# Kernel tuning notes

Hardware: AMD Instinct MI355X
Metric: run time of the kernel (lower is better)

Reference implementation:

```python
import jax, jax.numpy as jnp
import numpy as np

B, F, H, D, K = 16384, 4096, 512, 64, 512  # batch, feat, hidden, emb_dim, codebook size
M = H // D  # code positions per sample


def _leaky(h):
    return jnp.where(h > 0, h, 0.01 * h)


def setup_inputs() -> dict:
    key = jax.random.key(0)
    ks = jax.random.split(key, 16)
    lin = lambda k, i, o: jax.random.normal(k, (i, o), jnp.float32) * (1.0 / np.sqrt(i))
    return {
        "x": jax.random.uniform(ks[0], (B, F), jnp.float32),
        "We1": lin(ks[1], F, 256), "be1": jnp.zeros((256,), jnp.float32),
        "We2": lin(ks[2], 256, 128), "be2": jnp.zeros((128,), jnp.float32),
        "We3": lin(ks[3], 128, H), "be3": jnp.zeros((H,), jnp.float32),
        "Wd1": lin(ks[4], H, 128), "bd1": jnp.zeros((128,), jnp.float32),
        "Wd2": lin(ks[5], 128, 256), "bd2": jnp.zeros((256,), jnp.float32),
        "Wd3": lin(ks[6], 256, F), "bd3": jnp.zeros((F,), jnp.float32),
        "codebook": jax.random.normal(ks[7], (D, K), jnp.float32) * 0.02,  # (emb_dim, num_embeddings)
    }


def _nearest(z_e, codebook):
    # z_e: (B, D, M); codebook: (D, K). Squared-distance argmin over K.
    x2 = jnp.sum(z_e * z_e, axis=1)                       # (B, M)
    xw = jnp.einsum('bdm,dk->bmk', z_e, codebook)         # (B, M, K)
    w2 = jnp.sum(codebook * codebook, axis=0)             # (K,)
    idx = jnp.argmin(x2[..., None] - 2.0 * xw + w2, axis=-1)  # (B, M)
    quant = jnp.swapaxes(codebook.T[idx], 1, 2)           # (B, D, M)
    return quant, idx


def reference(x, We1, be1, We2, be2, We3, be3, Wd1, bd1, Wd2, bd2, Wd3, bd3, codebook):
    # encoder MLP
    h = _leaky(x @ We1 + be1)
    h = _leaky(h @ We2 + be2)
    h = _leaky(h @ We3 + be3)                             # (B, H)
    z_e = h.reshape(B, D, M)
    # emb(z_e, weight_sg=True): straight-through, weight detached
    quant_sg, idx = _nearest(z_e, jax.lax.stop_gradient(codebook))
    z_q = z_e + jax.lax.stop_gradient(quant_sg - z_e)
    # emb(z_e.detach()): grads (if any) flow to codebook via gather
    emb, _ = _nearest(jax.lax.stop_gradient(z_e), codebook)
    # decoder MLP
    g = _leaky(z_q.reshape(B, H) @ Wd1 + bd1)
    g = _leaky(g @ Wd2 + bd2)
    X_pred = jax.nn.sigmoid(g @ Wd3 + bd3)                # (B, F)
    return idx, z_e, z_q, emb, X_pred
```

## Files before the change

kernel.cpp:

```cpp
#include <hip/hip_runtime.h>
#include <cstdint>
#include <cstddef>


static constexpr int BB = 16384;

typedef __attribute__((ext_vector_type(8))) short short8;
typedef __attribute__((ext_vector_type(8))) _Float16 half8;
typedef __attribute__((ext_vector_type(4))) float f32x4;

__device__ __forceinline__ unsigned short f2bf(float f) {
    union { float f; uint32_t u; } v; v.f = f;
    uint32_t r = (v.u + 0x7FFFu + ((v.u >> 16) & 1u)) >> 16;
    return (unsigned short)r;
}

__device__ __forceinline__ void lds_barrier() {
    asm volatile("s_waitcnt lgkmcnt(0)" ::: "memory");
    __builtin_amdgcn_s_barrier();
    __builtin_amdgcn_sched_barrier(0);
}

__global__ __launch_bounds__(256) void combine_act(
    const float* __restrict__ part, int S, size_t MN,
    const float* __restrict__ bias, int N,
    float* __restrict__ outF)
{
    const size_t e = ((size_t)blockIdx.x * 256 + threadIdx.x) * 4;
    if (e >= MN) return;
    float4 s = *(const float4*)(part + e);
    for (int i = 1; i < S; i++) {
        const float4 p = *(const float4*)(part + (size_t)i * MN + e);
        s.x += p.x; s.y += p.y; s.z += p.z; s.w += p.w;
    }
    const int col = (int)(e & (size_t)(N - 1));
    const float4 bv = *(const float4*)(bias + col);
    float v0 = s.x + bv.x, v1 = s.y + bv.y, v2 = s.z + bv.z, v3 = s.w + bv.w;
    v0 = (v0 > 0.f) ? v0 : 0.01f * v0;
    v1 = (v1 > 0.f) ? v1 : 0.01f * v1;
    v2 = (v2 > 0.f) ? v2 : 0.01f * v2;
    v3 = (v3 > 0.f) ? v3 : 0.01f * v3;
    float4 o; o.x = v0; o.y = v1; o.z = v2; o.w = v3;
    *(float4*)(outF + e) = o;
}

__global__ __launch_bounds__(256) void transpose_cast(
    const float* __restrict__ W, unsigned short* __restrict__ WT, int R, int Cc)
{
    __shared__ float s[32][33];
    const int tx = threadIdx.x & 31, ty = threadIdx.x >> 5;
    const int c0 = blockIdx.x * 32, r0 = blockIdx.y * 32;
#pragma unroll
    for (int i = 0; i < 4; i++)
        s[ty + i * 8][tx] = W[(size_t)(r0 + ty + i * 8) * Cc + c0 + tx];
    __syncthreads();
#pragma unroll
    for (int i = 0; i < 4; i++)
        WT[(size_t)(c0 + ty + i * 8) * R + r0 + tx] = f2bf(s[tx][ty + i * 8]);
}

__global__ __launch_bounds__(256) void transpose_split_f16(
    const float* __restrict__ W, unsigned short* __restrict__ Th,
    unsigned short* __restrict__ Tl, int R, int Cc)
{
    __shared__ float s[32][33];
    const int tx = threadIdx.x & 31, ty = threadIdx.x >> 5;
    const int c0 = blockIdx.x * 32, r0 = blockIdx.y * 32;
#pragma unroll
    for (int i = 0; i < 4; i++)
        s[ty + i * 8][tx] = W[(size_t)(r0 + ty + i * 8) * Cc + c0 + tx];
    __syncthreads();
#pragma unroll
    for (int i = 0; i < 4; i++) {
        const float f = s[tx][ty + i * 8];
        const _Float16 h = (_Float16)f;
        const float fh = (float)h;
        const _Float16 lo = (_Float16)((f - fh) * 4096.0f);
        union { _Float16 hf; unsigned short u; } ch, cl;
        ch.hf = h; cl.hf = lo;
        Th[(size_t)(c0 + ty + i * 8) * R + r0 + tx] = ch.u;
        Tl[(size_t)(c0 + ty + i * 8) * R + r0 + tx] = cl.u;
    }
}

template<int BUF>
__device__ __forceinline__ void enc1_step(
    int K0,
    const float* __restrict__ gA,
    const unsigned short* __restrict__ gBh,
    const unsigned short* __restrict__ gBl,
    short (&Ah)[2][2048], short (&Al)[2][2048],
    half8 (&bhC)[4], half8 (&bhN)[4], half8 (&blS)[4],
    f32x4& p0, f32x4& p1,
    f32x4 (&acc1)[4][4], f32x4 (&acc2)[4][4],
    int aoff, int fr0)
{
    constexpr size_t rstep = (size_t)16 * 4096;
    const int kn1 = K0 + 32, kn2 = K0 + 64;
    lds_barrier();
#pragma unroll
    for (int j = 0; j < 4; j++)
        blS[j] = *(const half8*)(gBl + (size_t)j * rstep + K0);
    if (kn1 < 2048) {
#pragma unroll
        for (int j = 0; j < 4; j++)
            bhN[j] = *(const half8*)(gBh + (size_t)j * rstep + kn1);
    }
    f32x4 f0, f1;
    if (kn2 < 2048) {
        f0 = __builtin_nontemporal_load((const f32x4*)(gA + kn2));
        f1 = __builtin_nontemporal_load((const f32x4*)(gA + kn2 + 4));
    }
    half8 ah[4];
#pragma unroll
    for (int i = 0; i < 4; i++)
        ah[i] = *(const half8*)&Ah[BUF][(i << 9) + fr0];
#pragma unroll
    for (int i = 0; i < 4; i++)
#pragma unroll
        for (int j = 0; j < 4; j++)
            acc1[i][j] = __builtin_amdgcn_mfma_f32_16x16x32_f16(
                ah[i], bhC[j], acc1[i][j], 0, 0, 0);
#pragma unroll
    for (int i = 0; i < 4; i++)
#pragma unroll
        for (int j = 0; j < 4; j++)
            acc2[i][j] = __builtin_amdgcn_mfma_f32_16x16x32_f16(
                ah[i], blS[j], acc2[i][j], 0, 0, 0);
    half8 al[4];
#pragma unroll
    for (int i = 0; i < 4; i++)
        al[i] = *(const half8*)&Al[BUF][(i << 9) + fr0];
#pragma unroll
    for (int i = 0; i < 4; i++)
#pragma unroll
        for (int j = 0; j < 4; j++)
            acc2[i][j] = __builtin_amdgcn_mfma_f32_16x16x32_f16(
                al[i], bhC[j], acc2[i][j], 0, 0, 0);
    if (kn1 < 2048) {
        float fv[8];
        *(f32x4*)&fv[0] = p0;
        *(f32x4*)&fv[4] = p1;
        union { _Float16 h[8]; short8 s; } uh, ul;
#pragma unroll
        for (int e = 0; e < 8; e++) {
            const float f = fv[e];
            const _Float16 h = (_Float16)f;
            const float fh = (float)h;
            uh.h[e] = h;
            ul.h[e] = (_Float16)((f - fh) * 4096.0f);
        }
        *(short8*)&Ah[BUF ^ 1][aoff] = uh.s;
        *(short8*)&Al[BUF ^ 1][aoff] = ul.s;
    }
    if (kn2 < 2048) { p0 = f0; p1 = f1; }
}

__global__ __launch_bounds__(256, 2) void gemm_f16x2_enc1(
    const float* __restrict__ X,
    const unsigned short* __restrict__ Bh,
    const unsigned short* __restrict__ Bl,
    float* __restrict__ part)
{
    __shared__ short Ah[2][2048];
    __shared__ short Al[2][2048];
    const int tid = threadIdx.x;
    const int l = tid & 63, w = tid >> 6;
    const int lm = l & 15, lq = l >> 4;
    const int bm = blockIdx.y * 64;
    const int kStart = blockIdx.z * 2048;

    const float* gA = X + (size_t)(bm + w * 16 + lm) * 4096 + kStart + lq * 8;
    const unsigned short* gBh = Bh + (size_t)(w * 64 + lm) * 4096 + kStart + lq * 8;
    const unsigned short* gBl = Bl + (size_t)(w * 64 + lm) * 4096 + kStart + lq * 8;
    constexpr size_t rstep = (size_t)16 * 4096;

    const int aoff = (w << 9) + (l << 3);
    const int fr0 = (lq << 7) + (lm << 3);

    f32x4 acc1[4][4], acc2[4][4];
#pragma unroll
    for (int i = 0; i < 4; i++)
#pragma unroll
        for (int j = 0; j < 4; j++) {
            acc1[i][j] = (f32x4){0.f, 0.f, 0.f, 0.f};
            acc2[i][j] = (f32x4){0.f, 0.f, 0.f, 0.f};
        }

    half8 bhA[4], bhB[4], blS[4];
    f32x4 p0, p1;

    {
#pragma unroll
        for (int j = 0; j < 4; j++)
            bhA[j] = *(const half8*)(gBh + (size_t)j * rstep);
        f32x4 a0 = __builtin_nontemporal_load((const f32x4*)(gA));
        f32x4 a1 = __builtin_nontemporal_load((const f32x4*)(gA + 4));
        p0 = __builtin_nontemporal_load((const f32x4*)(gA + 32));
        p1 = __builtin_nontemporal_load((const f32x4*)(gA + 36));
        float fv[8];
        *(f32x4*)&fv[0] = a0;
        *(f32x4*)&fv[4] = a1;
        union { _Float16 h[8]; short8 s; } uh, ul;
#pragma unroll
        for (int e = 0; e < 8; e++) {
            const float f = fv[e];
            const _Float16 h = (_Float16)f;
            const float fh = (float)h;
            uh.h[e] = h;
            ul.h[e] = (_Float16)((f - fh) * 4096.0f);
        }
        *(short8*)&Ah[0][aoff] = uh.s;
        *(short8*)&Al[0][aoff] = ul.s;
    }

    for (int k2 = 0; k2 < 2048; k2 += 64) {
        enc1_step<0>(k2,      gA, gBh, gBl, Ah, Al, bhA, bhB, blS,
                     p0, p1, acc1, acc2, aoff, fr0);
        enc1_step<1>(k2 + 32, gA, gBh, gBl, Ah, Al, bhB, bhA, blS,
                     p0, p1, acc1, acc2, aoff, fr0);
    }

    float* P = part + (size_t)blockIdx.z * BB * 256;
    const float inv = 0.000244140625f;
#pragma unroll
    for (int i = 0; i < 4; i++)
#pragma unroll
        for (int j = 0; j < 4; j++) {
            const int col = w * 64 + j * 16 + lm;
#pragma unroll
            for (int r = 0; r < 4; r++) {
                const int row = bm + i * 16 + lq * 4 + r;
                P[(size_t)row * 256 + col] = acc1[i][j][r] + inv * acc2[i][j][r];
            }
        }
}

template<int BUF, int NJ, int KLEN>
__device__ __forceinline__ void mid_step(
    int K0,
    const float* __restrict__ gA,
    const unsigned short* __restrict__ gBh,
    const unsigned short* __restrict__ gBl,
    short (&Ah)[2][2048], short (&Al)[2][2048],
    half8 (&bhC)[NJ], half8 (&bhN)[NJ], half8 (&blS)[NJ],
    f32x4& p0, f32x4& p1,
    f32x4 (&acc1)[4][NJ], f32x4 (&acc2)[4][NJ],
    int aoff, int fr0)
{
    constexpr size_t rstep = (size_t)16 * KLEN;
    const int kn1 = K0 + 32, kn2 = K0 + 64;
    lds_barrier();
#pragma unroll
    for (int j = 0; j < NJ; j++)
        blS[j] = *(const half8*)(gBl + (size_t)j * rstep + K0);
    if (kn1 < KLEN) {
#pragma unroll
        for (int j = 0; j < NJ; j++)
            bhN[j] = *(const half8*)(gBh + (size_t)j * rstep + kn1);
    }
    f32x4 f0, f1;
    if (kn2 < KLEN) {
        f0 = *(const f32x4*)(gA + kn2);
        f1 = *(const f32x4*)(gA + kn2 + 4);
    }
    half8 ah[4];
#pragma unroll
    for (int i = 0; i < 4; i++)
        ah[i] = *(const half8*)&Ah[BUF][(i << 9) + fr0];
#pragma unroll
    for (int i = 0; i < 4; i++)
#pragma unroll
        for (int j = 0; j < NJ; j++)
            acc1[i][j] = __builtin_amdgcn_mfma_f32_16x16x32_f16(
                ah[i], bhC[j], acc1[i][j], 0, 0, 0);
#pragma unroll
    for (int i = 0; i < 4; i++)
#pragma unroll
        for (int j = 0; j < NJ; j++)
            acc2[i][j] = __builtin_amdgcn_mfma_f32_16x16x32_f16(
                ah[i], blS[j], acc2[i][j], 0, 0, 0);
    half8 al[4];
#pragma unroll
    for (int i = 0; i < 4; i++)
        al[i] = *(const half8*)&Al[BUF][(i << 9) + fr0];
#pragma unroll
    for (int i = 0; i < 4; i++)
#pragma unroll
        for (int j = 0; j < NJ; j++)
            acc2[i][j] = __builtin_amdgcn_mfma_f32_16x16x32_f16(
                al[i], bhC[j], acc2[i][j], 0, 0, 0);
    if (kn1 < KLEN) {
        float fv[8];
        *(f32x4*)&fv[0] = p0;
        *(f32x4*)&fv[4] = p1;
        union { _Float16 h[8]; short8 s; } uh, ul;
#pragma unroll
        for (int e = 0; e < 8; e++) {
            const float f = fv[e];
            const _Float16 h = (_Float16)f;
            const float fh = (float)h;
            uh.h[e] = h;
            ul.h[e] = (_Float16)((f - fh) * 4096.0f);
        }
        *(short8*)&Ah[BUF ^ 1][aoff] = uh.s;
        *(short8*)&Al[BUF ^ 1][aoff] = ul.s;
    }
    if (kn2 < KLEN) { p0 = f0; p1 = f1; }
}

template<int NJ, int KLEN, int ACT>
__global__ __launch_bounds__(256, 2) void gemm_f16x2_mid(
    const float* __restrict__ A,
    const unsigned short* __restrict__ Bh,
    const unsigned short* __restrict__ Bl,
    const float* __restrict__ bias,
    float* __restrict__ Cf, unsigned short* __restrict__ Cb)
{
    __shared__ short Ah[2][2048];
    __shared__ short Al[2][2048];
    const int tid = threadIdx.x;
    const int l = tid & 63, w = tid >> 6;
    const int lm = l & 15, lq = l >> 4;
    const int bm = blockIdx.y * 64;
    const int bn = blockIdx.x * (64 * NJ);
    const int N = gridDim.x * 64 * NJ;

    const float* gA = A + (size_t)(bm + w * 16 + lm) * KLEN + lq * 8;
    const unsigned short* gBh = Bh + (size_t)(bn + w * (16 * NJ) + lm) * KLEN + lq * 8;
    const unsigned short* gBl = Bl + (size_t)(bn + w * (16 * NJ) + lm) * KLEN + lq * 8;
    constexpr size_t rstep = (size_t)16 * KLEN;

    const int aoff = (w << 9) + (l << 3);
    const int fr0 = (lq << 7) + (lm << 3);

    f32x4 acc1[4][NJ], acc2[4][NJ];
#pragma unroll
    for (int i = 0; i < 4; i++)
#pragma unroll
        for (int j = 0; j < NJ; j++) {
            acc1[i][j] = (f32x4){0.f, 0.f, 0.f, 0.f};
            acc2[i][j] = (f32x4){0.f, 0.f, 0.f, 0.f};
        }

    half8 bhA[NJ], bhB[NJ], blS[NJ];
    f32x4 p0, p1;

    {
#pragma unroll
        for (int j = 0; j < NJ; j++)
            bhA[j] = *(const half8*)(gBh + (size_t)j * rstep);
        f32x4 a0 = *(const f32x4*)(gA);
        f32x4 a1 = *(const f32x4*)(gA + 4);
        p0 = *(const f32x4*)(gA + 32);
        p1 = *(const f32x4*)(gA + 36);
        float fv[8];
        *(f32x4*)&fv[0] = a0;
        *(f32x4*)&fv[4] = a1;
        union { _Float16 h[8]; short8 s; } uh, ul;
#pragma unroll
        for (int e = 0; e < 8; e++) {
            const float f = fv[e];
            const _Float16 h = (_Float16)f;
            const float fh = (float)h;
            uh.h[e] = h;
            ul.h[e] = (_Float16)((f - fh) * 4096.0f);
        }
        *(short8*)&Ah[0][aoff] = uh.s;
        *(short8*)&Al[0][aoff] = ul.s;
    }

    for (int k2 = 0; k2 < KLEN; k2 += 64) {
        mid_step<0, NJ, KLEN>(k2,      gA, gBh, gBl, Ah, Al, bhA, bhB, blS,
                              p0, p1, acc1, acc2, aoff, fr0);
        mid_step<1, NJ, KLEN>(k2 + 32, gA, gBh, gBl, Ah, Al, bhB, bhA, blS,
                              p0, p1, acc1, acc2, aoff, fr0);
    }

    const float inv = 0.000244140625f;
#pragma unroll
    for (int i = 0; i < 4; i++)
#pragma unroll
        for (int j = 0; j < NJ; j++) {
            const int col = bn + w * (16 * NJ) + j * 16 + lm;
            const float bv = bias[col];
#pragma unroll
            for (int r = 0; r < 4; r++) {
                const int row = bm + i * 16 + lq * 4 + r;
                float v = acc1[i][j][r] + inv * acc2[i][j][r] + bv;
                v = (v > 0.f) ? v : 0.01f * v;
                if (ACT == 0) Cf[(size_t)row * N + col] = v;
                else          Cb[(size_t)row * N + col] = f2bf(v);
            }
        }
}

__device__ __forceinline__ void dec3_step(
    int kn,
    const unsigned short* __restrict__ gA,
    const unsigned short* __restrict__ gB,
    short8 (&afC)[4], short8 (&bfC)[4],
    short8 (&afN)[4], short8 (&bfN)[4],
    f32x4 (&acc)[4][4])
{
    if (kn < 256) {
#pragma unroll
        for (int i = 0; i < 4; i++)
            afN[i] = *(const short8*)(gA + (size_t)i * 16 * 256 + kn);
#pragma unroll
        for (int j = 0; j < 4; j++)
            bfN[j] = *(const short8*)(gB + (size_t)j * 16 * 256 + kn);
    }
#pragma unroll
    for (int i = 0; i < 4; i++)
#pragma unroll
        for (int j = 0; j < 4; j++)
            acc[i][j] = __builtin_amdgcn_mfma_f32_16x16x32_bf16(
                afC[i], bfC[j], acc[i][j], 0, 0, 0);
}

__global__ __launch_bounds__(256) void gemm_bf16_dec3(
    const unsigned short* __restrict__ Ag,
    const unsigned short* __restrict__ Bt,
    const float* __restrict__ bias, float* __restrict__ C)
{
    const int tid = threadIdx.x;
    const int l = tid & 63, w = tid >> 6;
    const int lm = l & 15, lq = l >> 4;
    const int bm = blockIdx.y * 128, bn = blockIdx.x * 128;
    const int wm = (w >> 1) * 64, wn = (w & 1) * 64;

    const unsigned short* gA = Ag + (size_t)(bm + wm + lm) * 256 + lq * 8;
    const unsigned short* gB = Bt + (size_t)(bn + wn + lm) * 256 + lq * 8;

    f32x4 acc[4][4];
#pragma unroll
    for (int i = 0; i < 4; i++)
#pragma unroll
        for (int j = 0; j < 4; j++) acc[i][j] = (f32x4){0.f, 0.f, 0.f, 0.f};

    short8 afA[4], afB[4], bfA[4], bfB[4];
#pragma unroll
    for (int i = 0; i < 4; i++)
        afA[i] = *(const short8*)(gA + (size_t)i * 16 * 256);
#pragma unroll
    for (int j = 0; j < 4; j++)
        bfA[j] = *(const short8*)(gB + (size_t)j * 16 * 256);

    for (int k0 = 0; k0 < 256; k0 += 64) {
        dec3_step(k0 + 32, gA, gB, afA, bfA, afB, bfB, acc);
        dec3_step(k0 + 64, gA, gB, afB, bfB, afA, bfA, acc);
    }

#pragma unroll
    for (int i = 0; i < 4; i++) {
#pragma unroll
        for (int j = 0; j < 4; j++) {
            const int col = bn + wn + j * 16 + lm;
            const float bv = bias[col];
#pragma unroll
            for (int r = 0; r < 4; r++) {
                const int row = bm + wm + i * 16 + lq * 4 + r;
                float v = acc[i][j][r] + bv;
                v = 1.0f / (1.0f + __expf(-v));
                C[(size_t)row * 4096 + col] = v;
            }
        }
    }
}

__global__ __launch_bounds__(512) void vq_argmin(
    const float* __restrict__ ze, const float* __restrict__ cb,
    float* __restrict__ idxf, float* __restrict__ zq, float* __restrict__ emb)
{
    __shared__ float cbs[64 * 516];
    __shared__ float As[64][68];
    __shared__ float w2s[512];
    __shared__ int ids[64];
    const int tid = threadIdx.x;
    const int p0 = blockIdx.x * 64;

    const float4* cb4 = (const float4*)cb;
    float4* cbs4 = (float4*)cbs;
    for (int i = tid; i < 8192; i += 512)
        cbs4[(i >> 7) * 129 + (i & 127)] = cb4[i];

    const float4* ze4 = (const float4*)(ze + (size_t)p0 * 64);
    for (int i = tid; i < 1024; i += 512) {
        float4 v = ze4[i];
        int e = i * 4;
        int bo = e >> 9, r = e & 511;
        int d = r >> 3, m = r & 7;
        *(float4*)&As[d][bo * 8 + m] = v;
    }
    __syncthreads();

    {
        float s = 0.f;
#pragma unroll
        for (int d = 0; d < 64; ++d) { float c = cbs[d * 516 + tid]; s = fmaf(c, c, s); }
        w2s[tid] = s;
    }
    __syncthreads();

    const int tx = tid & 63;
    const int ty = tid >> 6;

    float acc[8][8], x2a[8];
#pragma unroll
    for (int i = 0; i < 8; i++) {
        x2a[i] = 0.f;
#pragma unroll
        for (int j = 0; j < 8; j++) acc[i][j] = 0.f;
    }

#pragma unroll 8
    for (int kk = 0; kk < 64; ++kk) {
        float a[8], b[8];
        *(float4*)&a[0] = *(const float4*)&As[kk][ty * 8];
        *(float4*)&a[4] = *(const float4*)&As[kk][ty * 8 + 4];
#pragma unroll
        for (int j = 0; j < 8; j++) b[j] = cbs[kk * 516 + tx + j * 64];
#pragma unroll
        for (int i = 0; i < 8; i++) x2a[i] = fmaf(a[i], a[i], x2a[i]);
#pragma unroll
        for (int i = 0; i < 8; i++)
#pragma unroll
            for (int j = 0; j < 8; j++)
                acc[i][j] = fmaf(a[i], b[j], acc[i][j]);
    }

    float w2v[8];
#pragma unroll
    for (int j = 0; j < 8; j++) w2v[j] = w2s[tx + j * 64];

#pragma unroll
    for (int i = 0; i < 8; i++) {
        float bd = 3.4e38f; int bk = 1 << 30;
#pragma unroll
        for (int j = 0; j < 8; j++) {
            float dsc = (x2a[i] - 2.0f * acc[i][j]) + w2v[j];
            int kc = tx + j * 64;
            if (dsc < bd || (dsc == bd && kc < bk)) { bd = dsc; bk = kc; }
        }
        for (int off = 32; off > 0; off >>= 1) {
            float od = __shfl_xor(bd, off);
            int   ok = __shfl_xor(bk, off);
            if (od < bd || (od == bd && ok < bk)) { bd = od; bk = ok; }
        }
        if (tx == i) {
            idxf[p0 + ty * 8 + i] = (float)bk;
            ids[ty * 8 + i] = bk;
        }
    }

    __syncthreads();
    const int bl_ = tid >> 6, dd = tid & 63;
    const int kbase = bl_ * 8;
    float zq8[8], em8[8];
#pragma unroll
    for (int mm = 0; mm < 8; mm++) {
        const int k = ids[kbase + mm];
        const float q = cbs[dd * 516 + k];
        const float z = As[dd][kbase + mm];
        em8[mm] = q;
        zq8[mm] = z + (q - z);
    }
    float* zqp = zq + (size_t)p0 * 64 + bl_ * 512 + dd * 8;
    float* emp = emb + (size_t)p0 * 64 + bl_ * 512 + dd * 8;
    *(float4*)zqp = *(float4*)&zq8[0];
    *(float4*)(zqp + 4) = *(float4*)&zq8[4];
    *(float4*)emp = *(float4*)&em8[0];
    *(float4*)(emp + 4) = *(float4*)&em8[4];
}

extern "C" void kernel_launch(void* const* d_in, const int* in_sizes, int n_in,
                              void* d_out, int out_size, void* d_ws, size_t ws_size,
                              hipStream_t stream)
{
    const float* x   = (const float*)d_in[0];
    const float* We1 = (const float*)d_in[1];
    const float* be1 = (const float*)d_in[2];
    const float* We2 = (const float*)d_in[3];
    const float* be2 = (const float*)d_in[4];
    const float* We3 = (const float*)d_in[5];
    const float* be3 = (const float*)d_in[6];
    const float* Wd1 = (const float*)d_in[7];
    const float* bd1 = (const float*)d_in[8];
    const float* Wd2 = (const float*)d_in[9];
    const float* bd2 = (const float*)d_in[10];
    const float* Wd3 = (const float*)d_in[11];
    const float* bd3 = (const float*)d_in[12];
    const float* cb  = (const float*)d_in[13];

    float* out   = (float*)d_out;
    float* o_idx = out;
    float* o_ze  = o_idx + 131072;
    float* o_zq  = o_ze + 8388608;
    float* o_emb = o_zq + 8388608;
    float* o_X   = o_emb + 8388608;

    float* h1 = (float*)d_ws;
    float* h2 = h1 + (size_t)BB * 256;
    float* g1 = h1;
    unsigned short* g2b = (unsigned short*)(h1 + (size_t)BB * 128);
    unsigned short* WT  = (unsigned short*)h2;

    unsigned short* Bth  = (unsigned short*)(o_X + 16777216);
    unsigned short* Btl  = Bth + 1048576;
    unsigned short* W2h  = Btl + 1048576;
    unsigned short* W2l  = W2h + 32768;
    unsigned short* W3h  = W2l + 32768;
    unsigned short* W3l  = W3h + 65536;
    unsigned short* Wd1h = W3l + 65536;
    unsigned short* Wd1l = Wd1h + 65536;
    unsigned short* Wd2h = Wd1l + 65536;
    unsigned short* Wd2l = Wd2h + 32768;

    transpose_split_f16<<<dim3(8, 128), 256, 0, stream>>>(We1, Bth, Btl, 4096, 256);
    transpose_split_f16<<<dim3(4, 8),   256, 0, stream>>>(We2, W2h, W2l, 256, 128);
    transpose_split_f16<<<dim3(16, 4),  256, 0, stream>>>(We3, W3h, W3l, 128, 512);
    transpose_split_f16<<<dim3(4, 16),  256, 0, stream>>>(Wd1, Wd1h, Wd1l, 512, 128);
    transpose_split_f16<<<dim3(8, 4),   256, 0, stream>>>(Wd2, Wd2h, Wd2l, 128, 256);

    gemm_f16x2_enc1<<<dim3(1, 256, 2), 256, 0, stream>>>(x, Bth, Btl, o_X);
    combine_act<<<4096, 256, 0, stream>>>(o_X, 2, (size_t)BB * 256, be1, 256, h1);
    gemm_f16x2_mid<2, 256, 0><<<dim3(1, 256), 256, 0, stream>>>(
        h1, W2h, W2l, be2, h2, nullptr);
    gemm_f16x2_mid<4, 128, 0><<<dim3(2, 256), 256, 0, stream>>>(
        h2, W3h, W3l, be3, o_ze, nullptr);

    transpose_cast<<<dim3(128, 8), 256, 0, stream>>>(Wd3, WT, 256, 4096);

    vq_argmin<<<dim3(2048), dim3(512), 0, stream>>>(o_ze, cb, o_idx, o_zq, o_emb);

    gemm_f16x2_mid<2, 512, 0><<<dim3(1, 256), 256, 0, stream>>>(
        o_zq, Wd1h, Wd1l, bd1, g1, nullptr);
    gemm_f16x2_mid<4, 128, 1><<<dim3(1, 256), 256, 0, stream>>>(
        g1, Wd2h, Wd2l, bd2, nullptr, g2b);
    gemm_bf16_dec3<<<dim3(32, 128), 256, 0, stream>>>(g2b, WT, bd3, o_X);
}
```

Baseline: 1.033 ms.

## Move VQ nearest-codebook search onto split-fp16 MFMA with precomputed codebook norms

Replaces the scalar-FMA VQ argmin kernel with an MFMA version. The z_e tile and a pre-transposed codebook are split into fp16 high and low parts to emulate fp32 dot products. Codebook squared norms are computed once in a small separate kernel instead of in every block, and the x2 term is dropped because it does not change the argmin. Each block now handles 32 positions and no longer stages the whole codebook in LDS. Codebook fragments are read from global memory per wave instead. The split-fp16 dot products may break near-ties slightly differently than fp32.

```diff
diff --git a/kernel.cpp b/kernel.cpp
--- a/kernel.cpp
+++ b/kernel.cpp
@@ -81,6 +81,15 @@
         Th[(size_t)(c0 + ty + i * 8) * R + r0 + tx] = ch.u;
         Tl[(size_t)(c0 + ty + i * 8) * R + r0 + tx] = cl.u;
     }
+}
+
+__global__ __launch_bounds__(512) void cb_w2(
+    const float* __restrict__ cb, float* __restrict__ w2g)
+{
+    const int k = threadIdx.x;
+    float s = 0.f;
+    for (int d = 0; d < 64; d++) { float c = cb[d * 512 + k]; s = fmaf(c, c, s); }
+    w2g[k] = s;
 }
 
 template<int BUF>
@@ -469,109 +478,182 @@
     }
 }
 
-__global__ __launch_bounds__(512) void vq_argmin(
+__global__ __launch_bounds__(256) void vq_mfma(
     const float* __restrict__ ze, const float* __restrict__ cb,
+    const unsigned short* __restrict__ cbTh,
+    const unsigned short* __restrict__ cbTl,
+    const float* __restrict__ w2g,
     float* __restrict__ idxf, float* __restrict__ zq, float* __restrict__ emb)
 {
-    __shared__ float cbs[64 * 516];
-    __shared__ float As[64][68];
-    __shared__ float w2s[512];
-    __shared__ int ids[64];
+    __shared__ short Ahh[2048], All[2048];
+    __shared__ float As[64][33];
+    __shared__ float redv[32][4];
+    __shared__ int   redk[32][4];
+    __shared__ int   kq[32];
     const int tid = threadIdx.x;
-    const int p0 = blockIdx.x * 64;
-
-    const float4* cb4 = (const float4*)cb;
-    float4* cbs4 = (float4*)cbs;
-    for (int i = tid; i < 8192; i += 512)
-        cbs4[(i >> 7) * 129 + (i & 127)] = cb4[i];
-
-    const float4* ze4 = (const float4*)(ze + (size_t)p0 * 64);
-    for (int i = tid; i < 1024; i += 512) {
-        float4 v = ze4[i];
-        int e = i * 4;
-        int bo = e >> 9, r = e & 511;
-        int d = r >> 3, m = r & 7;
-        *(float4*)&As[d][bo * 8 + m] = v;
+    const int l = tid & 63, w = tid >> 6;
+    const int lm = l & 15, lq = l >> 4;
+    const int b0 = blockIdx.x * 4;
+
+    const unsigned short* gBh = cbTh + (size_t)(w * 128 + lm) * 64 + lq * 8;
+    const unsigned short* gBl = cbTl + (size_t)(w * 128 + lm) * 64 + lq * 8;
+    half8 bh[8], bl[8];
+#pragma unroll
+    for (int j = 0; j < 8; j++) {
+        bh[j] = *(const half8*)(gBh + (size_t)j * 1024);
+        bl[j] = *(const half8*)(gBl + (size_t)j * 1024);
+    }
+
+#pragma unroll
+    for (int ff = 0; ff < 2; ff++) {
+        const int e = (tid + ff * 256) * 4;
+        const int s = e >> 9, r = e & 511, d = r >> 3, m = r & 7;
+        const f32x4 v = *(const f32x4*)(ze + (size_t)b0 * 512 + e);
+#pragma unroll
+        for (int c = 0; c < 4; c++) {
+            const float fv = v[c];
+            const int row = s * 8 + m + c;
+            As[d][row] = fv;
+            const _Float16 h = (_Float16)fv;
+            const float fh = (float)h;
+            const _Float16 lo = (_Float16)((fv - fh) * 4096.0f);
+            union { _Float16 hf; unsigned short u; } ch, cl;
+            ch.hf = h; cl.hf = lo;
+            const int off = (row >> 4) * 1024 + (d >> 5) * 512 +
+                            ((d >> 3) & 3) * 128 + (row & 15) * 8 + (d & 7);
+            Ahh[off] = (short)ch.u;
+            All[off] = (short)cl.u;
+        }
     }
     __syncthreads();
 
+    f32x4 acc1[2][8], acc2[2][8];
+#pragma unroll
+    for (int i = 0; i < 2; i++)
+#pragma unroll
+        for (int j = 0; j < 8; j++) {
+            acc1[i][j] = (f32x4){0.f, 0.f, 0.f, 0.f};
+            acc2[i][j] = (f32x4){0.f, 0.f, 0.f, 0.f};
+        }
+
+    const int fr0 = lq * 128 + lm * 8;
+    half8 ah0[2], al0[2];
+#pragma unroll
+    for (int i = 0; i < 2; i++) {
+        ah0[i] = *(const half8*)&Ahh[i * 1024 + fr0];
+        al0[i] = *(const half8*)&All[i * 1024 + fr0];
+    }
+#pragma unroll
+    for (int i = 0; i < 2; i++)
+#pragma unroll
+        for (int j = 0; j < 8; j++)
+            acc1[i][j] = __builtin_amdgcn_mfma_f32_16x16x32_f16(
+                ah0[i], bh[j], acc1[i][j], 0, 0, 0);
+#pragma unroll
+    for (int i = 0; i < 2; i++)
+#pragma unroll
+        for (int j = 0; j < 8; j++)
+            acc2[i][j] = __builtin_amdgcn_mfma_f32_16x16x32_f16(
+                al0[i], bh[j], acc2[i][j], 0, 0, 0);
+#pragma unroll
+    for (int j = 0; j < 8; j++) {
+        half8 nb = *(const half8*)(gBh + (size_t)j * 1024 + 32);
+#pragma unroll
+        for (int i = 0; i < 2; i++)
+            acc2[i][j] = __builtin_amdgcn_mfma_f32_16x16x32_f16(
+                ah0[i], bl[j], acc2[i][j], 0, 0, 0);
+        bh[j] = nb;
+    }
+#pragma unroll
+    for (int j = 0; j < 8; j++)
+        bl[j] = *(const half8*)(gBl + (size_t)j * 1024 + 32);
+    half8 ah1[2], al1[2];
+#pragma unroll
+    for (int i = 0; i < 2; i++) {
+        ah1[i] = *(const half8*)&Ahh[i * 1024 + 512 + fr0];
+        al1[i] = *(const half8*)&All[i * 1024 + 512 + fr0];
+    }
+#pragma unroll
+    for (int i = 0; i < 2; i++)
+#pragma unroll
+        for (int j = 0; j < 8; j++)
+            acc1[i][j] = __builtin_amdgcn_mfma_f32_16x16x32_f16(
+                ah1[i], bh[j], acc1[i][j], 0, 0, 0);
+#pragma unroll
+    for (int i = 0; i < 2; i++)
+#pragma unroll
+        for (int j = 0; j < 8; j++)
+            acc2[i][j] = __builtin_amdgcn_mfma_f32_16x16x32_f16(
+                ah1[i], bl[j], acc2[i][j], 0, 0, 0);
+#pragma unroll
+    for (int i = 0; i < 2; i++)
+#pragma unroll
+        for (int j = 0; j < 8; j++)
+            acc2[i][j] = __builtin_amdgcn_mfma_f32_16x16x32_f16(
+                al1[i], bh[j], acc2[i][j], 0, 0, 0);
+
+    const float inv = 0.000244140625f;
+    float w2v[8];
+#pragma unroll
+    for (int j = 0; j < 8; j++) w2v[j] = w2g[w * 128 + j * 16 + lm];
+
+#pragma unroll
+    for (int i = 0; i < 2; i++)
+#pragma unroll
+        for (int r = 0; r < 4; r++) {
+            float bd = 3.4e38f; int bk = 1 << 30;
+#pragma unroll
+            for (int j = 0; j < 8; j++) {
+                const float s = acc1[i][j][r] + inv * acc2[i][j][r];
+                const float dsc = w2v[j] - 2.0f * s;
+                const int kc = w * 128 + j * 16 + lm;
+                if (dsc < bd || (dsc == bd && kc < bk)) { bd = dsc; bk = kc; }
+            }
+#pragma unroll
+            for (int off = 1; off < 16; off <<= 1) {
+                const float od = __shfl_xor(bd, off);
+                const int   ok = __shfl_xor(bk, off);
+                if (od < bd || (od == bd && ok < bk)) { bd = od; bk = ok; }
+            }
+            if (lm == 0) {
+                const int row = i * 16 + lq * 4 + r;
+                redv[row][w] = bd;
+                redk[row][w] = bk;
+            }
+        }
+    __syncthreads();
+
+    if (tid < 32) {
+        float bd = redv[tid][0]; int bk = redk[tid][0];
+#pragma unroll
+        for (int ww = 1; ww < 4; ww++) {
+            const float od = redv[tid][ww];
+            const int   ok = redk[tid][ww];
+            if (od < bd || (od == bd && ok < bk)) { bd = od; bk = ok; }
+        }
+        idxf[(size_t)b0 * 8 + tid] = (float)bk;
+        kq[tid] = bk;
+    }
+    __syncthreads();
+
     {
-        float s = 0.f;
-#pragma unroll
-        for (int d = 0; d < 64; ++d) { float c = cbs[d * 516 + tid]; s = fmaf(c, c, s); }
-        w2s[tid] = s;
-    }
-    __syncthreads();
-
-    const int tx = tid & 63;
-    const int ty = tid >> 6;
-
-    float acc[8][8], x2a[8];
-#pragma unroll
-    for (int i = 0; i < 8; i++) {
-        x2a[i] = 0.f;
-#pragma unroll
-        for (int j = 0; j < 8; j++) acc[i][j] = 0.f;
-    }
-
-#pragma unroll 8
-    for (int kk = 0; kk < 64; ++kk) {
-        float a[8], b[8];
-        *(float4*)&a[0] = *(const float4*)&As[kk][ty * 8];
-        *(float4*)&a[4] = *(const float4*)&As[kk][ty * 8 + 4];
-#pragma unroll
-        for (int j = 0; j < 8; j++) b[j] = cbs[kk * 516 + tx + j * 64];
-#pragma unroll
-        for (int i = 0; i < 8; i++) x2a[i] = fmaf(a[i], a[i], x2a[i]);
-#pragma unroll
-        for (int i = 0; i < 8; i++)
-#pragma unroll
-            for (int j = 0; j < 8; j++)
-                acc[i][j] = fmaf(a[i], b[j], acc[i][j]);
-    }
-
-    float w2v[8];
-#pragma unroll
-    for (int j = 0; j < 8; j++) w2v[j] = w2s[tx + j * 64];
-
-#pragma unroll
-    for (int i = 0; i < 8; i++) {
-        float bd = 3.4e38f; int bk = 1 << 30;
-#pragma unroll
-        for (int j = 0; j < 8; j++) {
-            float dsc = (x2a[i] - 2.0f * acc[i][j]) + w2v[j];
-            int kc = tx + j * 64;
-            if (dsc < bd || (dsc == bd && kc < bk)) { bd = dsc; bk = kc; }
-        }
-        for (int off = 32; off > 0; off >>= 1) {
-            float od = __shfl_xor(bd, off);
-            int   ok = __shfl_xor(bk, off);
-            if (od < bd || (od == bd && ok < bk)) { bd = od; bk = ok; }
-        }
-        if (tx == i) {
-            idxf[p0 + ty * 8 + i] = (float)bk;
-            ids[ty * 8 + i] = bk;
-        }
-    }
-
-    __syncthreads();
-    const int bl_ = tid >> 6, dd = tid & 63;
-    const int kbase = bl_ * 8;
-    float zq8[8], em8[8];
-#pragma unroll
-    for (int mm = 0; mm < 8; mm++) {
-        const int k = ids[kbase + mm];
-        const float q = cbs[dd * 516 + k];
-        const float z = As[dd][kbase + mm];
-        em8[mm] = q;
-        zq8[mm] = z + (q - z);
-    }
-    float* zqp = zq + (size_t)p0 * 64 + bl_ * 512 + dd * 8;
-    float* emp = emb + (size_t)p0 * 64 + bl_ * 512 + dd * 8;
-    *(float4*)zqp = *(float4*)&zq8[0];
-    *(float4*)(zqp + 4) = *(float4*)&zq8[4];
-    *(float4*)emp = *(float4*)&em8[0];
-    *(float4*)(emp + 4) = *(float4*)&em8[4];
+        const int ss = tid >> 6, dd = tid & 63;
+        float zq8[8], em8[8];
+#pragma unroll
+        for (int mm = 0; mm < 8; mm++) {
+            const int k = kq[ss * 8 + mm];
+            const float q = cb[dd * 512 + k];
+            const float z = As[dd][ss * 8 + mm];
+            em8[mm] = q;
+            zq8[mm] = z + (q - z);
+        }
+        float* zqp = zq + (size_t)(b0 + ss) * 512 + dd * 8;
+        float* emp = emb + (size_t)(b0 + ss) * 512 + dd * 8;
+        *(float4*)zqp = *(float4*)&zq8[0];
+        *(float4*)(zqp + 4) = *(float4*)&zq8[4];
+        *(float4*)emp = *(float4*)&em8[0];
+        *(float4*)(emp + 4) = *(float4*)&em8[4];
+    }
 }
 
 extern "C" void kernel_launch(void* const* d_in, const int* in_sizes, int n_in,
@@ -616,12 +698,17 @@
     unsigned short* Wd1l = Wd1h + 65536;
     unsigned short* Wd2h = Wd1l + 65536;
     unsigned short* Wd2l = Wd2h + 32768;
+    unsigned short* cbTh = Wd2l + 32768;
+    unsigned short* cbTl = cbTh + 32768;
+    float*          w2g  = (float*)(cbTl + 32768);
 
     transpose_split_f16<<<dim3(8, 128), 256, 0, stream>>>(We1, Bth, Btl, 4096, 256);
     transpose_split_f16<<<dim3(4, 8),   256, 0, stream>>>(We2, W2h, W2l, 256, 128);
     transpose_split_f16<<<dim3(16, 4),  256, 0, stream>>>(We3, W3h, W3l, 128, 512);
     transpose_split_f16<<<dim3(4, 16),  256, 0, stream>>>(Wd1, Wd1h, Wd1l, 512, 128);
     transpose_split_f16<<<dim3(8, 4),   256, 0, stream>>>(Wd2, Wd2h, Wd2l, 128, 256);
+    transpose_split_f16<<<dim3(16, 2),  256, 0, stream>>>(cb, cbTh, cbTl, 64, 512);
+    cb_w2<<<dim3(1), dim3(512), 0, stream>>>(cb, w2g);
 
     gemm_f16x2_enc1<<<dim3(1, 256, 2), 256, 0, stream>>>(x, Bth, Btl, o_X);
     combine_act<<<4096, 256, 0, stream>>>(o_X, 2, (size_t)BB * 256, be1, 256, h1);
@@ -632,7 +719,8 @@
 
     transpose_cast<<<dim3(128, 8), 256, 0, stream>>>(Wd3, WT, 256, 4096);
 
-    vq_argmin<<<dim3(2048), dim3(512), 0, stream>>>(o_ze, cb, o_idx, o_zq, o_emb);
+    vq_mfma<<<dim3(4096), dim3(256), 0, stream>>>(
+        o_ze, cb, cbTh, cbTl, w2g, o_idx, o_zq, o_emb);
 
     gemm_f16x2_mid<2, 512, 0><<<dim3(1, 256), 256, 0, stream>>>(
         o_zq, Wd1h, Wd1l, bd1, g1, nullptr);
```

New measurement: 1.021 ms. No clear change (-1.1%).
